# Optimization experiments

Measured on AMD Instinct MI355X. Metric: run time of the kernel, lower is better.

## Reference

```python
import jax, jax.numpy as jnp
import numpy as np

N, NFEAT, NHID1, NHID2, NCLASS = 16384, 512, 256, 128, 8


def setup_inputs() -> dict:
    key = jax.random.key(0)
    ks = jax.random.split(key, 8)
    x = jax.random.normal(ks[0], (N, NFEAT), dtype=jnp.float32)
    adj = jax.random.uniform(ks[1], (N, N), dtype=jnp.float32)
    W1 = jax.random.normal(ks[2], (NFEAT, NHID1), dtype=jnp.float32) * (1.0 / np.sqrt(NFEAT))
    b1 = jnp.zeros((NHID1,), dtype=jnp.float32)
    W2 = jax.random.normal(ks[3], (NHID1, NHID2), dtype=jnp.float32) * (1.0 / np.sqrt(NHID1))
    b2 = jnp.zeros((NHID2,), dtype=jnp.float32)
    W3 = jax.random.normal(ks[4], (NHID2, NCLASS), dtype=jnp.float32) * (1.0 / np.sqrt(NHID2))
    b3 = jnp.zeros((NCLASS,), dtype=jnp.float32)
    return {"x": x, "adj": adj, "W1": W1, "b1": b1, "W2": W2, "b2": b2, "W3": W3, "b3": b3}


def _gc(x, adj, W, b):
    # GraphConvolution (Kipf): support = x @ W; out = adj @ support + b
    return adj @ (x @ W) + b


def reference(x, adj, W1, b1, W2, b2, W3, b3):
    # eval mode: dropout is identity
    h = jax.nn.relu(_gc(x, adj, W1, b1))
    h = jax.nn.relu(_gc(h, adj, W2, b2))
    h = _gc(h, adj, W3, b3)
    return jax.nn.log_softmax(h, axis=1)
```

## Files before the change

### kernel.cpp

```cpp
#include <hip/hip_runtime.h>
#include <hip/hip_bf16.h>

#define NROW 16384
#define NFEATC 512
#define NH1 256
#define NH2 128
#define NCLS 8

typedef __attribute__((ext_vector_type(8))) short short8;
typedef __attribute__((ext_vector_type(4))) float f32x4;

__device__ __forceinline__ ushort f2bf(float f) {
  union { float f; unsigned u; } v; v.f = f;
  unsigned r = v.u + 0x7FFFu + ((v.u >> 16) & 1u);
  return (ushort)(r >> 16);
}
__device__ __forceinline__ float bf2f(ushort h) {
  union { unsigned u; float f; } v; v.u = ((unsigned)h) << 16; return v.f;
}

__global__ __launch_bounds__(256) void transpose_conv(
    const float* __restrict__ in, ushort* __restrict__ out, int K, int N) {
  int idx = blockIdx.x * 256 + threadIdx.x;
  if (idx < K * N) {
    int k = idx / N, n = idx % N;
    out[(size_t)n * K + k] = f2bf(in[idx]);
  }
}

template<int BM, int BN, int WM, int WN, int KSPLIT, bool AFP32, int OUTM>
__global__ __launch_bounds__(256, 2) void gemm_pipe(
    const void* __restrict__ Ap, const ushort* __restrict__ BT,
    void* __restrict__ Outp, const int nm, const int nn,
    const int M, const int N, const int K)
{
  constexpr int BK = 64, LDSK = BK + 8;
  constexpr int MR = WM / 16, NR = WN / 16;
  constexpr int nWc = BN / WN;
  static_assert((BM / WM) * (BN / WN) == 4, "4 waves");
  constexpr int AELEM = BM * BK / 256, ATPR = BK / AELEM;
  constexpr int BELEM = BN * BK / 256, BTPR = BK / BELEM;
  constexpr int A4 = AELEM / 4, A8 = AELEM / 8, B8 = BELEM / 8;

  __shared__ ushort As[2][BM * LDSK];
  __shared__ ushort Bs[2][BN * LDSK];

  const int t = threadIdx.x, l = t & 63, wid = t >> 6;
  const int wr0 = (wid / nWc) * WM, wc0 = (wid % nWc) * WN;

  const int cpx = gridDim.x >> 3;
  const int flat = (blockIdx.x & 7) * cpx + (blockIdx.x >> 3);
  const int n_blk = flat % nn;
  const int m_blk = (flat / nn) % nm;
  const int ksl = flat / (nn * nm);
  const int bm0 = m_blk * BM, bn0 = n_blk * BN;
  const int kper = K / KSPLIT;
  const int kbase = ksl * kper;
  const int NT = kper / BK;

  const int ar = t / ATPR, ak = (t % ATPR) * AELEM;
  const int br = t / BTPR, bk = (t % BTPR) * BELEM;

  const float*  Af = (const float*)Ap + (size_t)(bm0 + ar) * K + kbase + ak;
  const ushort* Ab = (const ushort*)Ap + (size_t)(bm0 + ar) * K + kbase + ak;
  const ushort* Bp = BT + (size_t)(bn0 + br) * K + kbase + bk;

  float4 aF[AFP32 ? A4 : 1];
  short8 aB8[AFP32 ? 1 : A8];
  short8 bB8[B8];
  f32x4 acc[MR][NR] = {};

  auto loadRegs = [&](int it) {
    const int ko = it * BK;
    if constexpr (AFP32) {
      #pragma unroll
      for (int c = 0; c < A4; c++) aF[c] = *(const float4*)(Af + ko + 4 * c);
    } else {
      #pragma unroll
      for (int c = 0; c < A8; c++) aB8[c] = *(const short8*)(Ab + ko + 8 * c);
    }
    #pragma unroll
    for (int c = 0; c < B8; c++) bB8[c] = *(const short8*)(Bp + ko + 8 * c);
  };
  auto writeLds = [&](int buf) {
    if constexpr (AFP32) {
      #pragma unroll
      for (int c = 0; c < A4; c++) {
        ushort4 v;
        v.x = f2bf(aF[c].x); v.y = f2bf(aF[c].y);
        v.z = f2bf(aF[c].z); v.w = f2bf(aF[c].w);
        *(ushort4*)&As[buf][ar * LDSK + ak + 4 * c] = v;
      }
    } else {
      #pragma unroll
      for (int c = 0; c < A8; c++)
        *(short8*)&As[buf][ar * LDSK + ak + 8 * c] = aB8[c];
    }
    #pragma unroll
    for (int c = 0; c < B8; c++)
      *(short8*)&Bs[buf][br * LDSK + bk + 8 * c] = bB8[c];
  };
  auto compute = [&](int buf) {
    const int rr = l & 15;
    #pragma unroll
    for (int kk = 0; kk < 2; kk++) {
      const int kb = kk * 32 + (l >> 4) * 8;
      short8 af[MR], bfv[NR];
      #pragma unroll
      for (int m = 0; m < MR; m++)
        af[m] = *(short8*)&As[buf][(wr0 + m * 16 + rr) * LDSK + kb];
      #pragma unroll
      for (int n = 0; n < NR; n++)
        bfv[n] = *(short8*)&Bs[buf][(wc0 + n * 16 + rr) * LDSK + kb];
      #pragma unroll
      for (int m = 0; m < MR; m++)
        #pragma unroll
        for (int n = 0; n < NR; n++)
          acc[m][n] = __builtin_amdgcn_mfma_f32_16x16x32_bf16(af[m], bfv[n], acc[m][n], 0, 0, 0);
    }
  };

  loadRegs(0);
  writeLds(0);
  __syncthreads();
  for (int it = 0; it < NT; it++) {
    const int cur = it & 1;
    if (it + 1 < NT) loadRegs(it + 1);
    compute(cur);
    if (it + 1 < NT) writeLds(cur ^ 1);
    __syncthreads();
  }

  #pragma unroll
  for (int m = 0; m < MR; m++) {
    const int row = bm0 + wr0 + m * 16 + (l >> 4) * 4;
    #pragma unroll
    for (int n = 0; n < NR; n++) {
      const int col = bn0 + wc0 + n * 16 + (l & 15);
      if constexpr (OUTM == 1) {
        ushort4 v;
        v.x = f2bf(acc[m][n][0]); v.y = f2bf(acc[m][n][1]);
        v.z = f2bf(acc[m][n][2]); v.w = f2bf(acc[m][n][3]);
        *(ushort4*)((ushort*)Outp + (size_t)col * M + row) = v;
      } else {
        float* o = (float*)Outp + (size_t)ksl * M * N;
        #pragma unroll
        for (int r = 0; r < 4; r++)
          o[(size_t)(row + r) * N + col] = acc[m][n][r];
      }
    }
  }
}

__global__ __launch_bounds__(256) void reduce_relu(
    const float* __restrict__ part, const float* __restrict__ bias,
    ushort* __restrict__ out, const int MN, const int N, const int KS) {
  const int i4 = (blockIdx.x * 256 + threadIdx.x) * 4;
  if (i4 >= MN) return;
  float4 s = *(const float4*)(part + i4);
  for (int k = 1; k < KS; k++) {
    float4 p = *(const float4*)(part + (size_t)k * MN + i4);
    s.x += p.x; s.y += p.y; s.z += p.z; s.w += p.w;
  }
  const int col = i4 % N;
  float4 b = *(const float4*)(bias + col);
  ushort4 v;
  v.x = f2bf(fmaxf(s.x + b.x, 0.0f));
  v.y = f2bf(fmaxf(s.y + b.y, 0.0f));
  v.z = f2bf(fmaxf(s.z + b.z, 0.0f));
  v.w = f2bf(fmaxf(s.w + b.w, 0.0f));
  *(ushort4*)(out + i4) = v;
}

__global__ __launch_bounds__(256) void mm_small(
    const ushort* __restrict__ h2, const float* __restrict__ W3,
    ushort* __restrict__ s3T) {
  __shared__ float w[NH2 * NCLS];
  for (int i = threadIdx.x; i < NH2 * NCLS; i += 256) w[i] = W3[i];
  __syncthreads();
  const int m = blockIdx.x * 256 + threadIdx.x;
  float acc[8] = {};
  const ushort* row = h2 + (size_t)m * NH2;
  #pragma unroll
  for (int c = 0; c < NH2 / 8; c++) {
    short8 v = *(const short8*)(row + c * 8);
    #pragma unroll
    for (int j = 0; j < 8; j++) {
      float h = bf2f((ushort)v[j]);
      const int k = c * 8 + j;
      #pragma unroll
      for (int n = 0; n < 8; n++) acc[n] += h * w[k * 8 + n];
    }
  }
  #pragma unroll
  for (int n = 0; n < 8; n++) s3T[(size_t)n * NROW + m] = f2bf(acc[n]);
  #pragma unroll
  for (int n = 8; n < 16; n++) s3T[(size_t)n * NROW + m] = 0;
}

__global__ __launch_bounds__(256, 2) void gemm_final(
    const float* __restrict__ adj, const ushort* __restrict__ s3T,
    float* __restrict__ part)
{
  constexpr int BM = 128, BK = 64, LDSK = BK + 8;
  __shared__ ushort As[2][BM * LDSK];
  const int t = threadIdx.x, l = t & 63, wid = t >> 6;
  const int wr0 = wid * 32;
  const int cpx = gridDim.x >> 3;
  const int flat = (blockIdx.x & 7) * cpx + (blockIdx.x >> 3);
  const int m_blk = flat & 127;
  const int ksl = flat >> 7;
  const int bm0 = m_blk * BM;
  const int kbase = ksl * (NROW / 4);
  constexpr int NT = (NROW / 4) / BK;
  const int ar = t >> 1, ak = (t & 1) * 32;
  const float* Af = adj + (size_t)(bm0 + ar) * NROW + kbase + ak;
  float4 aF[8];
  f32x4 acc[2] = {};

  auto loadA = [&](int it) {
    #pragma unroll
    for (int c = 0; c < 8; c++) aF[c] = *(const float4*)(Af + it * BK + 4 * c);
  };
  auto writeA = [&](int buf) {
    #pragma unroll
    for (int c = 0; c < 8; c++) {
      ushort4 v;
      v.x = f2bf(aF[c].x); v.y = f2bf(aF[c].y);
      v.z = f2bf(aF[c].z); v.w = f2bf(aF[c].w);
      *(ushort4*)&As[buf][ar * LDSK + ak + 4 * c] = v;
    }
  };
  const int rr = l & 15;
  auto comp = [&](int buf, int it) {
    #pragma unroll
    for (int kk = 0; kk < 2; kk++) {
      const int kb = kk * 32 + (l >> 4) * 8;
      short8 bfv = *(const short8*)(s3T + (size_t)rr * NROW + kbase + it * BK + kb);
      short8 af0 = *(short8*)&As[buf][(wr0 + rr) * LDSK + kb];
      short8 af1 = *(short8*)&As[buf][(wr0 + 16 + rr) * LDSK + kb];
      acc[0] = __builtin_amdgcn_mfma_f32_16x16x32_bf16(af0, bfv, acc[0], 0, 0, 0);
      acc[1] = __builtin_amdgcn_mfma_f32_16x16x32_bf16(af1, bfv, acc[1], 0, 0, 0);
    }
  };

  loadA(0); writeA(0); __syncthreads();
  for (int it = 0; it < NT; it++) {
    const int cur = it & 1;
    if (it + 1 < NT) loadA(it + 1);
    comp(cur, it);
    if (it + 1 < NT) writeA(cur ^ 1);
    __syncthreads();
  }

  float* op = part + (size_t)ksl * NROW * 16;
  #pragma unroll
  for (int m = 0; m < 2; m++) {
    const int row = bm0 + wr0 + m * 16 + (l >> 4) * 4;
    #pragma unroll
    for (int r = 0; r < 4; r++)
      op[(size_t)(row + r) * 16 + rr] = acc[m][r];
  }
}

__global__ __launch_bounds__(256) void final_reduce(
    const float* __restrict__ part, const float* __restrict__ b3,
    float* __restrict__ out) {
  const int m = blockIdx.x * 256 + threadIdx.x;
  float4 s0 = make_float4(0, 0, 0, 0), s1 = make_float4(0, 0, 0, 0);
  #pragma unroll
  for (int k = 0; k < 4; k++) {
    const float4* p = (const float4*)(part + ((size_t)k * NROW + m) * 16);
    float4 a = p[0], b = p[1];
    s0.x += a.x; s0.y += a.y; s0.z += a.z; s0.w += a.w;
    s1.x += b.x; s1.y += b.y; s1.z += b.z; s1.w += b.w;
  }
  float v[8];
  v[0] = s0.x + b3[0]; v[1] = s0.y + b3[1]; v[2] = s0.z + b3[2]; v[3] = s0.w + b3[3];
  v[4] = s1.x + b3[4]; v[5] = s1.y + b3[5]; v[6] = s1.z + b3[6]; v[7] = s1.w + b3[7];
  float mx = v[0];
  #pragma unroll
  for (int n = 1; n < 8; n++) mx = fmaxf(mx, v[n]);
  float s = 0.0f;
  #pragma unroll
  for (int n = 0; n < 8; n++) s += expf(v[n] - mx);
  const float lse = logf(s) + mx;
  float4* o = (float4*)(out + (size_t)m * 8);
  o[0] = make_float4(v[0] - lse, v[1] - lse, v[2] - lse, v[3] - lse);
  o[1] = make_float4(v[4] - lse, v[5] - lse, v[6] - lse, v[7] - lse);
}

extern "C" void kernel_launch(void* const* d_in, const int* in_sizes, int n_in,
                              void* d_out, int out_size, void* d_ws, size_t ws_size,
                              hipStream_t stream) {
  const float* x   = (const float*)d_in[0];
  const float* adj = (const float*)d_in[1];
  const float* W1  = (const float*)d_in[2];
  const float* b1  = (const float*)d_in[3];
  const float* W2  = (const float*)d_in[4];
  const float* b2  = (const float*)d_in[5];
  const float* W3  = (const float*)d_in[6];
  const float* b3  = (const float*)d_in[7];
  float* out = (float*)d_out;

  char* ws = (char*)d_ws;
  size_t off = 0;
  ushort* W1T = (ushort*)(ws + off); off += (size_t)NH1 * NFEATC * 2;
  ushort* W2T = (ushort*)(ws + off); off += (size_t)NH2 * NH1 * 2;
  ushort* s1T = (ushort*)(ws + off); off += (size_t)NH1 * NROW * 2;
  ushort* h1  = (ushort*)(ws + off); off += (size_t)NROW * NH1 * 2;
  ushort* s2T = (ushort*)(ws + off); off += (size_t)NH2 * NROW * 2;
  ushort* h2  = (ushort*)(ws + off); off += (size_t)NROW * NH2 * 2;
  ushort* s3T = (ushort*)(ws + off); off += (size_t)16 * NROW * 2;
  float*  part = (float*)(ws + off); off += (size_t)2 * NROW * NH1 * 4;

  transpose_conv<<<(NFEATC * NH1 + 255) / 256, 256, 0, stream>>>(W1, W1T, NFEATC, NH1);
  transpose_conv<<<(NH1 * NH2 + 255) / 256, 256, 0, stream>>>(W2, W2T, NH1, NH2);

  gemm_pipe<64, 128, 32, 64, 1, true, 1><<<512, 256, 0, stream>>>(
      x, W1T, s1T, 256, 2, NROW, NH1, NFEATC);
  gemm_pipe<128, 128, 64, 64, 2, true, 2><<<512, 256, 0, stream>>>(
      adj, s1T, part, 128, 2, NROW, NH1, NROW);
  reduce_relu<<<(NROW * NH1 / 4 + 255) / 256, 256, 0, stream>>>(
      part, b1, h1, NROW * NH1, NH1, 2);
  gemm_pipe<64, 128, 32, 64, 1, false, 1><<<256, 256, 0, stream>>>(
      h1, W2T, s2T, 256, 1, NROW, NH2, NH1);
  gemm_pipe<128, 128, 64, 64, 4, true, 2><<<512, 256, 0, stream>>>(
      adj, s2T, part, 128, 1, NROW, NH2, NROW);
  reduce_relu<<<(NROW * NH2 / 4 + 255) / 256, 256, 0, stream>>>(
      part, b2, h2, NROW * NH2, NH2, 4);
  mm_small<<<NROW / 256, 256, 0, stream>>>(h2, W3, s3T);
  gemm_final<<<512, 256, 0, stream>>>(adj, s3T, part);
  final_reduce<<<NROW / 256, 256, 0, stream>>>(part, b3, out);
}
```

Baseline: 862.2 us.

## Cache bf16 copy of adj in first pass and reuse it for later layers

The first adj GEMM now also writes a bf16 copy of adj to workspace, from the n_blk==0 blocks only. The second and third adj GEMMs read this half-size copy instead of re-reading and converting the fp32 adjacency, and the custom final kernel is replaced by a generic gemm_pipe instance with BN=16. The pipeline is also restructured with two register sets and an unrolled-by-two loop, and the second adj pass walks K in reverse to reuse recently written data in cache. This adds a 512MB extra write and workspace in exchange for halving reads in two passes. It also relies on the loop handling odd NT correctly.

```diff
diff --git a/kernel.cpp b/kernel.cpp
--- a/kernel.cpp
+++ b/kernel.cpp
@@ -28,11 +28,11 @@
   }
 }
 
-template<int BM, int BN, int WM, int WN, int KSPLIT, bool AFP32, int OUTM>
-__global__ __launch_bounds__(256, 2) void gemm_pipe(
+template<int BM, int BN, int WM, int WN, int KSPLIT, bool AFP32, int OUTM, bool KREV, int MINW>
+__global__ __launch_bounds__(256, MINW) void gemm_pipe(
     const void* __restrict__ Ap, const ushort* __restrict__ BT,
-    void* __restrict__ Outp, const int nm, const int nn,
-    const int M, const int N, const int K)
+    void* __restrict__ Outp, ushort* __restrict__ adjBF,
+    const int nm, const int nn, const int M, const int N, const int K)
 {
   constexpr int BK = 64, LDSK = BK + 8;
   constexpr int MR = WM / 16, NR = WN / 16;
@@ -40,7 +40,9 @@
   static_assert((BM / WM) * (BN / WN) == 4, "4 waves");
   constexpr int AELEM = BM * BK / 256, ATPR = BK / AELEM;
   constexpr int BELEM = BN * BK / 256, BTPR = BK / BELEM;
-  constexpr int A4 = AELEM / 4, A8 = AELEM / 8, B8 = BELEM / 8;
+  constexpr int A4s = AFP32 ? AELEM / 4 : 1;
+  constexpr int A8s = AFP32 ? 1 : AELEM / 8;
+  constexpr int B8s = (BELEM >= 8) ? BELEM / 8 : 1;
 
   __shared__ ushort As[2][BM * LDSK];
   __shared__ ushort Bs[2][BN * LDSK];
@@ -54,8 +56,7 @@
   const int m_blk = (flat / nn) % nm;
   const int ksl = flat / (nn * nm);
   const int bm0 = m_blk * BM, bn0 = n_blk * BN;
-  const int kper = K / KSPLIT;
-  const int kbase = ksl * kper;
+  const int kper = K / KSPLIT, kbase = ksl * kper;
   const int NT = kper / BK;
 
   const int ar = t / ATPR, ak = (t % ATPR) * AELEM;
@@ -64,42 +65,55 @@
   const float*  Af = (const float*)Ap + (size_t)(bm0 + ar) * K + kbase + ak;
   const ushort* Ab = (const ushort*)Ap + (size_t)(bm0 + ar) * K + kbase + ak;
   const ushort* Bp = BT + (size_t)(bn0 + br) * K + kbase + bk;
-
-  float4 aF[AFP32 ? A4 : 1];
-  short8 aB8[AFP32 ? 1 : A8];
-  short8 bB8[B8];
+  ushort* adjW = adjBF ? (adjBF + (size_t)(bm0 + ar) * K + kbase + ak) : nullptr;
+  const bool wbf = AFP32 && (adjW != nullptr) && (n_blk == 0);
+
   f32x4 acc[MR][NR] = {};
 
-  auto loadRegs = [&](int it) {
-    const int ko = it * BK;
+  auto loadRegs = [&](float4 (&aF)[A4s], short8 (&aB)[A8s],
+                      short8 (&bV)[B8s], ushort4& b4, int it) {
+    const int ko = (KREV ? (NT - 1 - it) : it) * BK;
     if constexpr (AFP32) {
       #pragma unroll
-      for (int c = 0; c < A4; c++) aF[c] = *(const float4*)(Af + ko + 4 * c);
-    } else {
-      #pragma unroll
-      for (int c = 0; c < A8; c++) aB8[c] = *(const short8*)(Ab + ko + 8 * c);
-    }
-    #pragma unroll
-    for (int c = 0; c < B8; c++) bB8[c] = *(const short8*)(Bp + ko + 8 * c);
+      for (int c = 0; c < A4s; c++) aF[c] = *(const float4*)(Af + ko + 4 * c);
+    } else {
+      #pragma unroll
+      for (int c = 0; c < A8s; c++) aB[c] = *(const short8*)(Ab + ko + 8 * c);
+    }
+    if constexpr (BELEM >= 8) {
+      #pragma unroll
+      for (int c = 0; c < B8s; c++) bV[c] = *(const short8*)(Bp + ko + 8 * c);
+    } else {
+      b4 = *(const ushort4*)(Bp + ko);
+    }
   };
-  auto writeLds = [&](int buf) {
+
+  auto writeLds = [&](int buf, float4 (&aF)[A4s], short8 (&aB)[A8s],
+                      short8 (&bV)[B8s], ushort4& b4, int it) {
+    const int ko = (KREV ? (NT - 1 - it) : it) * BK;
     if constexpr (AFP32) {
       #pragma unroll
-      for (int c = 0; c < A4; c++) {
+      for (int c = 0; c < A4s; c++) {
         ushort4 v;
         v.x = f2bf(aF[c].x); v.y = f2bf(aF[c].y);
         v.z = f2bf(aF[c].z); v.w = f2bf(aF[c].w);
         *(ushort4*)&As[buf][ar * LDSK + ak + 4 * c] = v;
+        if (wbf) *(ushort4*)(adjW + ko + 4 * c) = v;
       }
     } else {
       #pragma unroll
-      for (int c = 0; c < A8; c++)
-        *(short8*)&As[buf][ar * LDSK + ak + 8 * c] = aB8[c];
-    }
-    #pragma unroll
-    for (int c = 0; c < B8; c++)
-      *(short8*)&Bs[buf][br * LDSK + bk + 8 * c] = bB8[c];
+      for (int c = 0; c < A8s; c++)
+        *(short8*)&As[buf][ar * LDSK + ak + 8 * c] = aB[c];
+    }
+    if constexpr (BELEM >= 8) {
+      #pragma unroll
+      for (int c = 0; c < B8s; c++)
+        *(short8*)&Bs[buf][br * LDSK + bk + 8 * c] = bV[c];
+    } else {
+      *(ushort4*)&Bs[buf][br * LDSK + bk] = b4;
+    }
   };
+
   auto compute = [&](int buf) {
     const int rr = l & 15;
     #pragma unroll
@@ -120,14 +134,24 @@
     }
   };
 
-  loadRegs(0);
-  writeLds(0);
+  float4 XaF[A4s], YaF[A4s];
+  short8 XaB[A8s], YaB[A8s];
+  short8 XbV[B8s], YbV[B8s];
+  ushort4 Xb4, Yb4;
+
+  loadRegs(XaF, XaB, XbV, Xb4, 0);
+  writeLds(0, XaF, XaB, XbV, Xb4, 0);
+  loadRegs(XaF, XaB, XbV, Xb4, 1);
   __syncthreads();
-  for (int it = 0; it < NT; it++) {
-    const int cur = it & 1;
-    if (it + 1 < NT) loadRegs(it + 1);
-    compute(cur);
-    if (it + 1 < NT) writeLds(cur ^ 1);
+
+  for (int it = 0; it < NT; it += 2) {
+    if (it + 2 < NT) loadRegs(YaF, YaB, YbV, Yb4, it + 2);
+    compute(0);
+    if (it + 1 < NT) writeLds(1, XaF, XaB, XbV, Xb4, it + 1);
+    __syncthreads();
+    if (it + 3 < NT) loadRegs(XaF, XaB, XbV, Xb4, it + 3);
+    if (it + 1 < NT) compute(1);
+    if (it + 2 < NT) writeLds(0, YaF, YaB, YbV, Yb4, it + 2);
     __syncthreads();
   }
 
@@ -198,71 +222,6 @@
   for (int n = 8; n < 16; n++) s3T[(size_t)n * NROW + m] = 0;
 }
 
-__global__ __launch_bounds__(256, 2) void gemm_final(
-    const float* __restrict__ adj, const ushort* __restrict__ s3T,
-    float* __restrict__ part)
-{
-  constexpr int BM = 128, BK = 64, LDSK = BK + 8;
-  __shared__ ushort As[2][BM * LDSK];
-  const int t = threadIdx.x, l = t & 63, wid = t >> 6;
-  const int wr0 = wid * 32;
-  const int cpx = gridDim.x >> 3;
-  const int flat = (blockIdx.x & 7) * cpx + (blockIdx.x >> 3);
-  const int m_blk = flat & 127;
-  const int ksl = flat >> 7;
-  const int bm0 = m_blk * BM;
-  const int kbase = ksl * (NROW / 4);
-  constexpr int NT = (NROW / 4) / BK;
-  const int ar = t >> 1, ak = (t & 1) * 32;
-  const float* Af = adj + (size_t)(bm0 + ar) * NROW + kbase + ak;
-  float4 aF[8];
-  f32x4 acc[2] = {};
-
-  auto loadA = [&](int it) {
-    #pragma unroll
-    for (int c = 0; c < 8; c++) aF[c] = *(const float4*)(Af + it * BK + 4 * c);
-  };
-  auto writeA = [&](int buf) {
-    #pragma unroll
-    for (int c = 0; c < 8; c++) {
-      ushort4 v;
-      v.x = f2bf(aF[c].x); v.y = f2bf(aF[c].y);
-      v.z = f2bf(aF[c].z); v.w = f2bf(aF[c].w);
-      *(ushort4*)&As[buf][ar * LDSK + ak + 4 * c] = v;
-    }
-  };
-  const int rr = l & 15;
-  auto comp = [&](int buf, int it) {
-    #pragma unroll
-    for (int kk = 0; kk < 2; kk++) {
-      const int kb = kk * 32 + (l >> 4) * 8;
-      short8 bfv = *(const short8*)(s3T + (size_t)rr * NROW + kbase + it * BK + kb);
-      short8 af0 = *(short8*)&As[buf][(wr0 + rr) * LDSK + kb];
-      short8 af1 = *(short8*)&As[buf][(wr0 + 16 + rr) * LDSK + kb];
-      acc[0] = __builtin_amdgcn_mfma_f32_16x16x32_bf16(af0, bfv, acc[0], 0, 0, 0);
-      acc[1] = __builtin_amdgcn_mfma_f32_16x16x32_bf16(af1, bfv, acc[1], 0, 0, 0);
-    }
-  };
-
-  loadA(0); writeA(0); __syncthreads();
-  for (int it = 0; it < NT; it++) {
-    const int cur = it & 1;
-    if (it + 1 < NT) loadA(it + 1);
-    comp(cur, it);
-    if (it + 1 < NT) writeA(cur ^ 1);
-    __syncthreads();
-  }
-
-  float* op = part + (size_t)ksl * NROW * 16;
-  #pragma unroll
-  for (int m = 0; m < 2; m++) {
-    const int row = bm0 + wr0 + m * 16 + (l >> 4) * 4;
-    #pragma unroll
-    for (int r = 0; r < 4; r++)
-      op[(size_t)(row + r) * 16 + rr] = acc[m][r];
-  }
-}
-
 __global__ __launch_bounds__(256) void final_reduce(
     const float* __restrict__ part, const float* __restrict__ b3,
     float* __restrict__ out) {
@@ -313,23 +272,25 @@
   ushort* h2  = (ushort*)(ws + off); off += (size_t)NROW * NH2 * 2;
   ushort* s3T = (ushort*)(ws + off); off += (size_t)16 * NROW * 2;
   float*  part = (float*)(ws + off); off += (size_t)2 * NROW * NH1 * 4;
+  ushort* adjBF = (ushort*)(ws + off); off += (size_t)NROW * NROW * 2;
 
   transpose_conv<<<(NFEATC * NH1 + 255) / 256, 256, 0, stream>>>(W1, W1T, NFEATC, NH1);
   transpose_conv<<<(NH1 * NH2 + 255) / 256, 256, 0, stream>>>(W2, W2T, NH1, NH2);
 
-  gemm_pipe<64, 128, 32, 64, 1, true, 1><<<512, 256, 0, stream>>>(
-      x, W1T, s1T, 256, 2, NROW, NH1, NFEATC);
-  gemm_pipe<128, 128, 64, 64, 2, true, 2><<<512, 256, 0, stream>>>(
-      adj, s1T, part, 128, 2, NROW, NH1, NROW);
+  gemm_pipe<64, 128, 32, 64, 1, true, 1, false, 2><<<512, 256, 0, stream>>>(
+      x, W1T, s1T, nullptr, 256, 2, NROW, NH1, NFEATC);
+  gemm_pipe<128, 128, 64, 64, 2, true, 2, false, 2><<<512, 256, 0, stream>>>(
+      adj, s1T, part, adjBF, 128, 2, NROW, NH1, NROW);
   reduce_relu<<<(NROW * NH1 / 4 + 255) / 256, 256, 0, stream>>>(
       part, b1, h1, NROW * NH1, NH1, 2);
-  gemm_pipe<64, 128, 32, 64, 1, false, 1><<<256, 256, 0, stream>>>(
-      h1, W2T, s2T, 256, 1, NROW, NH2, NH1);
-  gemm_pipe<128, 128, 64, 64, 4, true, 2><<<512, 256, 0, stream>>>(
-      adj, s2T, part, 128, 1, NROW, NH2, NROW);
+  gemm_pipe<64, 128, 32, 64, 1, false, 1, false, 2><<<256, 256, 0, stream>>>(
+      h1, W2T, s2T, nullptr, 256, 1, NROW, NH2, NH1);
+  gemm_pipe<128, 128, 64, 64, 4, false, 2, true, 2><<<512, 256, 0, stream>>>(
+      adjBF, s2T, part, nullptr, 128, 1, NROW, NH2, NROW);
   reduce_relu<<<(NROW * NH2 / 4 + 255) / 256, 256, 0, stream>>>(
       part, b2, h2, NROW * NH2, NH2, 4);
   mm_small<<<NROW / 256, 256, 0, stream>>>(h2, W3, s3T);
-  gemm_final<<<512, 256, 0, stream>>>(adj, s3T, part);
+  gemm_pipe<128, 16, 32, 16, 4, false, 2, false, 3><<<512, 256, 0, stream>>>(
+      adjBF, s3T, part, nullptr, 128, 1, NROW, 16, NROW);
   final_reduce<<<NROW / 256, 256, 0, stream>>>(part, b3, out);
 }
```

Measured after the change: 867.6 us. About the same (+0.6%).
